# Kernel tuning notes

Hardware: AMD Instinct MI355X
Metric: run time of the kernel (lower is better)

## Reference

```python
import jax, jax.numpy as jnp
import numpy as np

# ---- architecture constants (from init_kwargs) ----
HID = 1024          # hidden_size
HK, HV = 4, 8       # linear_num_key_heads, linear_num_value_heads
DK, DV = 128, 128   # linear_key_head_dim, linear_value_head_dim
KEY_DIM = HK * DK   # 512
VAL_DIM = HV * DV   # 1024
CONV_DIM = 2 * KEY_DIM + VAL_DIM  # q,k,v concat -> 2048
KCONV = 4
NEXP, TOPK, INTER = 8, 2, 512
EPS = 1e-6


def setup_inputs() -> dict:
    key = jax.random.key(0)
    ks = jax.random.split(key, 12)
    def lin(k, shape, fan_in):
        return jax.random.normal(k, shape, jnp.float32) * (fan_in ** -0.5)
    return {
        "hidden_states": jax.random.normal(ks[0], (1, 2048, HID), jnp.float32),
        "w_ln1": jnp.zeros((HID,), jnp.float32),            # zero-centered RMSNorm weight
        "w_ln2": jnp.zeros((HID,), jnp.float32),
        "W_qkvz": lin(ks[1], (HID, 2 * KEY_DIM + 2 * VAL_DIM), HID),
        "W_ba": lin(ks[2], (HID, 2 * HV), HID),
        "conv_w": jax.random.normal(ks[3], (CONV_DIM, KCONV), jnp.float32) * (KCONV ** -0.5),
        "dt_bias": jax.random.normal(ks[4], (HV,), jnp.float32) * 0.1,
        "A_log": jnp.log(jax.random.uniform(ks[5], (HV,), jnp.float32, 1.0, 16.0)),
        "gate_norm_w": jnp.ones((DV,), jnp.float32),
        "W_out": lin(ks[6], (VAL_DIM, HID), VAL_DIM),
        "W_router": lin(ks[7], (HID, NEXP), HID),
        "W_gate_e": lin(ks[8], (NEXP, HID, INTER), HID),
        "W_up_e": lin(ks[9], (NEXP, HID, INTER), HID),
        "W_down_e": lin(ks[10], (NEXP, INTER, HID), INTER),
    }


def zrms(x, w):
    # zero-centered RMSNorm: effective weight is (1 + w)
    v = jnp.mean(x * x, axis=-1, keepdims=True)
    return x * jax.lax.rsqrt(v + EPS) * (1.0 + w)


def causal_dwconv(x, w):
    # x: [B,S,C], w: [C,K] depthwise causal conv
    xp = jnp.pad(x, ((0, 0), (KCONV - 1, 0), (0, 0)))
    kern = w.T[:, None, :]  # [K, 1, C] (HIO)
    return jax.lax.conv_general_dilated(
        xp, kern, (1,), 'VALID',
        dimension_numbers=('NHC', 'HIO', 'NHC'),
        feature_group_count=CONV_DIM)


def gated_delta_rule(q, k, v, g, beta):
    # q,k: [B,S,HV,DK] (l2-normed, q scaled); v: [B,S,HV,DV]; g,beta: [B,S,HV]
    B = q.shape[0]
    S0 = jnp.zeros((B, HV, DK, DV), q.dtype)
    def step(S, inp):
        qt, kt, vt, gt, bt = inp
        S = S * jnp.exp(gt)[..., None, None]
        kv = jnp.einsum('bhk,bhkv->bhv', kt, S)
        delta = (vt - kv) * bt[..., None]
        S = S + jnp.einsum('bhk,bhv->bhkv', kt, delta)
        o = jnp.einsum('bhk,bhkv->bhv', qt, S)
        return S, o
    xs = tuple(jnp.moveaxis(a, 1, 0) for a in (q, k, v, g, beta))
    _, o = jax.lax.scan(step, S0, xs)
    return jnp.moveaxis(o, 0, 1)  # [B,S,HV,DV]


def reference(hidden_states, w_ln1, w_ln2, W_qkvz, W_ba, conv_w, dt_bias, A_log,
              gate_norm_w, W_out, W_router, W_gate_e, W_up_e, W_down_e):
    B, S, _ = hidden_states.shape
    # ---- gated deltanet sub-block ----
    resid = hidden_states
    x = zrms(hidden_states, w_ln1)
    qkvz = x @ W_qkvz
    q, k, v, z = jnp.split(qkvz, [KEY_DIM, 2 * KEY_DIM, 2 * KEY_DIM + VAL_DIM], axis=-1)
    b, a = jnp.split(x @ W_ba, 2, axis=-1)            # each [B,S,HV]
    beta = jax.nn.sigmoid(b)
    g = -jnp.exp(A_log) * jax.nn.softplus(a + dt_bias)
    mixed = jnp.concatenate([q, k, v], axis=-1)
    mixed = jax.nn.silu(causal_dwconv(mixed, conv_w))
    q, k, v = jnp.split(mixed, [KEY_DIM, 2 * KEY_DIM], axis=-1)
    q = q.reshape(B, S, HK, DK)
    k = k.reshape(B, S, HK, DK)
    v = v.reshape(B, S, HV, DV)
    rep = HV // HK
    q = jnp.repeat(q, rep, axis=2)
    k = jnp.repeat(k, rep, axis=2)
    q = q * jax.lax.rsqrt(jnp.sum(q * q, -1, keepdims=True) + EPS)
    k = k * jax.lax.rsqrt(jnp.sum(k * k, -1, keepdims=True) + EPS)
    q = q * (DK ** -0.5)
    core = gated_delta_rule(q, k, v, g, beta)         # [B,S,HV,DV]
    # gated RMSNorm (per value head) with silu(z) gate
    core = core * jax.lax.rsqrt(jnp.mean(core * core, -1, keepdims=True) + EPS) * gate_norm_w
    core = core * jax.nn.silu(z.reshape(B, S, HV, DV))
    h = resid + core.reshape(B, S, VAL_DIM) @ W_out
    # ---- MoE sub-block ----
    resid = h
    x = zrms(h, w_ln2)
    probs = jax.nn.softmax(x @ W_router, axis=-1)     # [B,S,E]
    topv, topi = jax.lax.top_k(probs, TOPK)
    topv = topv / jnp.sum(topv, -1, keepdims=True)
    route = jnp.sum(jax.nn.one_hot(topi, NEXP, dtype=x.dtype) * topv[..., None], axis=-2)
    gate_h = jnp.einsum('bsh,ehi->bsei', x, W_gate_e)
    up_h = jnp.einsum('bsh,ehi->bsei', x, W_up_e)
    exp_out = jnp.einsum('bsei,eih->bseh', jax.nn.silu(gate_h) * up_h, W_down_e)
    moe_out = jnp.einsum('bseh,bse->bsh', exp_out, route)
    return (resid + moe_out, topi)
```

## Files before the change

### kernel.cpp

```cpp
#include <hip/hip_runtime.h>

#define S 2048
#define HID 1024
#define HK 4
#define HV 8
#define DK 128
#define DV 128
#define KEY_DIM 512
#define VAL_DIM 1024
#define CONV_DIM 2048
#define QKVZ_N 3072
#define NEXP 8
#define INTER 512
#define EPS 1e-6f
#define CK 64
#define NC 32

typedef unsigned short u16;
typedef unsigned int u32;
typedef __attribute__((ext_vector_type(8))) short bf16x8;
typedef __attribute__((ext_vector_type(4))) float f32x4;

__device__ __forceinline__ u16 f2b(float f) {
  u32 u = __builtin_bit_cast(u32, f);
  u += 0x7fff + ((u >> 16) & 1);
  return (u16)(u >> 16);
}

__device__ __forceinline__ void gload16(const u16* g, u16* l) {
  __builtin_amdgcn_global_load_lds(
      (const __attribute__((address_space(1))) void*)g,
      (__attribute__((address_space(3))) void*)l, 16, 0, 0);
}

__global__ __launch_bounds__(256) void k_rms(const float* __restrict__ x,
                                             const float* __restrict__ w,
                                             float* __restrict__ out,
                                             u16* __restrict__ outb) {
  const int row = blockIdx.x;
  const int tid = threadIdx.x;
  const float* xr = x + (size_t)row * HID;
  float4 v = ((const float4*)xr)[tid];
  float ss = v.x*v.x + v.y*v.y + v.z*v.z + v.w*v.w;
  for (int m = 1; m < 64; m <<= 1) ss += __shfl_xor(ss, m);
  __shared__ float sred[4];
  if ((tid & 63) == 0) sred[tid >> 6] = ss;
  __syncthreads();
  float tot = sred[0] + sred[1] + sred[2] + sred[3];
  float scale = 1.0f / sqrtf(tot * (1.0f / HID) + EPS);
  float4 wv = ((const float4*)w)[tid];
  float4 o;
  o.x = v.x * scale * (1.0f + wv.x);
  o.y = v.y * scale * (1.0f + wv.y);
  o.z = v.z * scale * (1.0f + wv.z);
  o.w = v.w * scale * (1.0f + wv.w);
  ((float4*)(out + (size_t)row * HID))[tid] = o;
  u32 p0 = (u32)f2b(o.x) | ((u32)f2b(o.y) << 16);
  u32 p1 = (u32)f2b(o.z) | ((u32)f2b(o.w) << 16);
  *(uint2*)&outb[(size_t)row * HID + tid * 4] = make_uint2(p0, p1);
}

__global__ __launch_bounds__(256) void k_transp(const float* __restrict__ src,
                                                u16* __restrict__ dst,
                                                int K, int N) {
  __shared__ float t[32][33];
  const size_t bo = (size_t)blockIdx.z * K * N;
  src += bo; dst += bo;
  int n0 = blockIdx.x * 32, k0 = blockIdx.y * 32;
  int tx = threadIdx.x & 31, ty = threadIdx.x >> 5;
#pragma unroll
  for (int i = 0; i < 32; i += 8)
    t[ty + i][tx] = src[(size_t)(k0 + ty + i) * N + n0 + tx];
  __syncthreads();
#pragma unroll
  for (int i = 0; i < 32; i += 8)
    dst[(size_t)(n0 + ty + i) * K + k0 + tx] = f2b(t[tx][ty + i]);
}

__global__ __launch_bounds__(256) void k_sgemm2(const float* __restrict__ A,
                                                const float* __restrict__ B,
                                                const float* __restrict__ Cadd,
                                                float* __restrict__ C,
                                                int M, int N, int K) {
  __shared__ float As[16][132];
  __shared__ float Bs[16][132];
  const int tid = threadIdx.x;
  const int ty = tid >> 4, tx = tid & 15;
  const int m0 = blockIdx.y * 128, n0 = blockIdx.x * 128;
  const int ar = tid >> 1, ak = (tid & 1) * 8;
  const int br = tid >> 4, bc = (tid & 15) * 8;
  float acc[8][8] = {};
  for (int k0 = 0; k0 < K; k0 += 16) {
    float4 a0 = *(const float4*)&A[(size_t)(m0 + ar) * K + k0 + ak];
    float4 a1 = *(const float4*)&A[(size_t)(m0 + ar) * K + k0 + ak + 4];
    As[ak + 0][ar] = a0.x; As[ak + 1][ar] = a0.y;
    As[ak + 2][ar] = a0.z; As[ak + 3][ar] = a0.w;
    As[ak + 4][ar] = a1.x; As[ak + 5][ar] = a1.y;
    As[ak + 6][ar] = a1.z; As[ak + 7][ar] = a1.w;
    *(float4*)&Bs[br][bc]     = *(const float4*)&B[(size_t)(k0 + br) * N + n0 + bc];
    *(float4*)&Bs[br][bc + 4] = *(const float4*)&B[(size_t)(k0 + br) * N + n0 + bc + 4];
    __syncthreads();
#pragma unroll
    for (int kk = 0; kk < 16; ++kk) {
      float4 aA = *(const float4*)&As[kk][ty * 8];
      float4 aB = *(const float4*)&As[kk][ty * 8 + 4];
      float4 bA = *(const float4*)&Bs[kk][tx * 8];
      float4 bB = *(const float4*)&Bs[kk][tx * 8 + 4];
      float a[8] = {aA.x, aA.y, aA.z, aA.w, aB.x, aB.y, aB.z, aB.w};
      float b[8] = {bA.x, bA.y, bA.z, bA.w, bB.x, bB.y, bB.z, bB.w};
#pragma unroll
      for (int i = 0; i < 8; ++i)
#pragma unroll
        for (int j = 0; j < 8; ++j) acc[i][j] += a[i] * b[j];
    }
    __syncthreads();
  }
#pragma unroll
  for (int i = 0; i < 8; ++i) {
    size_t off = (size_t)(m0 + ty * 8 + i) * N + n0 + tx * 8;
    float4 o0 = {acc[i][0], acc[i][1], acc[i][2], acc[i][3]};
    float4 o1 = {acc[i][4], acc[i][5], acc[i][6], acc[i][7]};
    if (Cadd) {
      float4 c0 = *(const float4*)&Cadd[off];
      float4 c1 = *(const float4*)&Cadd[off + 4];
      o0.x += c0.x; o0.y += c0.y; o0.z += c0.z; o0.w += c0.w;
      o1.x += c1.x; o1.y += c1.y; o1.z += c1.z; o1.w += c1.w;
    }
    *(float4*)&C[off] = o0;
    *(float4*)&C[off + 4] = o1;
  }
}

__global__ __launch_bounds__(256) void k_ba(const float* __restrict__ x1,
                                            const float* __restrict__ Wba,
                                            float* __restrict__ ba) {
  const int t = blockIdx.x, tid = threadIdx.x;
  const int n = tid >> 4, kl = tid & 15;
  const float* xr = x1 + (size_t)t * HID;
  float s = 0.f;
  for (int k = kl; k < HID; k += 16) s += xr[k] * Wba[k * 16 + n];
  for (int m = 1; m < 16; m <<= 1) s += __shfl_xor(s, m);
  if (kl == 0) ba[t * 16 + n] = s;
}

__global__ __launch_bounds__(256) void k_bg(const float* __restrict__ ba,
                                            const float* __restrict__ dt_bias,
                                            const float* __restrict__ A_log,
                                            float* __restrict__ gb,
                                            float* __restrict__ beta) {
  int i = blockIdx.x * 256 + threadIdx.x;
  if (i >= S * HV) return;
  int t = i >> 3, h = i & 7;
  float b = ba[t * 16 + h];
  float a = ba[t * 16 + 8 + h];
  beta[i] = 1.f / (1.f + expf(-b));
  float x = a + dt_bias[h];
  float sp = fmaxf(x, 0.f) + log1pf(expf(-fabsf(x)));
  gb[i] = -expf(A_log[h]) * sp;
}

__global__ __launch_bounds__(256) void k_conv(const float* __restrict__ qkvz,
                                              const float* __restrict__ cw,
                                              float* __restrict__ conv) {
  int idx = blockIdx.x * 256 + threadIdx.x;
  int t = idx >> 11, c = idx & 2047;
  float4 w = ((const float4*)cw)[c];
  float acc = 0.f;
  if (t >= 3) {
    acc = qkvz[(size_t)(t - 3) * QKVZ_N + c] * w.x
        + qkvz[(size_t)(t - 2) * QKVZ_N + c] * w.y
        + qkvz[(size_t)(t - 1) * QKVZ_N + c] * w.z
        + qkvz[(size_t)(t    ) * QKVZ_N + c] * w.w;
  } else {
    if (t - 3 >= 0) acc += qkvz[(size_t)(t - 3) * QKVZ_N + c] * w.x;
    if (t - 2 >= 0) acc += qkvz[(size_t)(t - 2) * QKVZ_N + c] * w.y;
    if (t - 1 >= 0) acc += qkvz[(size_t)(t - 1) * QKVZ_N + c] * w.z;
    acc += qkvz[(size_t)t * QKVZ_N + c] * w.w;
  }
  conv[idx] = acc / (1.f + expf(-acc));
}

__global__ __launch_bounds__(512) void k_prep(const float* __restrict__ conv,
                                              float* __restrict__ qn,
                                              float* __restrict__ kn) {
// ... 131 lines not shown
      *(float4*)&Upre[cb * 8192 + (size_t)(t0 + i) * 128 + c0 + 4] = o1;
    }
  }
  {
    const int r0 = (tid >> 3) * 4, t0 = (tid & 7) * 8;
    float acc[4][8] = {};
    for (int j = 0; j < 64; ++j) {
      float s = sW[j];
      float kk[4];
#pragma unroll
      for (int i = 0; i < 4; ++i) kk[i] = KT[r0 + i][j] * s;
      float m[8];
#pragma unroll
      for (int t = 0; t < 8; ++t) m[t] = Mm[t0 + t][j];
#pragma unroll
      for (int i = 0; i < 4; ++i)
#pragma unroll
        for (int t = 0; t < 8; ++t) acc[i][t] += kk[i] * m[t];
    }
#pragma unroll
    for (int i = 0; i < 4; ++i) {
      float4 o0 = {acc[i][0], acc[i][1], acc[i][2], acc[i][3]};
      float4 o1 = {acc[i][4], acc[i][5], acc[i][6], acc[i][7]};
      *(float4*)&WpT[cb * 8192 + (size_t)(r0 + i) * 64 + t0] = o0;
      *(float4*)&WpT[cb * 8192 + (size_t)(r0 + i) * 64 + t0 + 4] = o1;
    }
  }
  __syncthreads();

  float* QT = UB;
#pragma unroll
  for (int i = 0; i < 8; ++i) {
    int w = (i * 256 + tid) * 4;
    int tt = w >> 7, r = w & 127;
    float4 v = *(const float4*)&qn[(size_t)(t_base + tt) * 1024 + h * 128 + r];
    QT[(r + 0) * 68 + tt] = v.x; QT[(r + 1) * 68 + tt] = v.y;
    QT[(r + 2) * 68 + tt] = v.z; QT[(r + 3) * 68 + tt] = v.w;
  }
  __syncthreads();

  {
    const int t0 = (tid >> 4) * 4, j0 = (tid & 15) * 4;
    float acc[4][4] = {};
    for (int r = 0; r < 128; ++r) {
      float4 a = *(const float4*)&QT[r * 68 + t0];
      float4 b = *(const float4*)&KT[r][j0];
      float av[4] = {a.x, a.y, a.z, a.w};
      float bv[4] = {b.x, b.y, b.z, b.w};
#pragma unroll
      for (int i = 0; i < 4; ++i)
#pragma unroll
        for (int j = 0; j < 4; ++j) acc[i][j] += av[i] * bv[j];
    }
#pragma unroll
    for (int i = 0; i < 4; ++i)
#pragma unroll
      for (int j = 0; j < 4; ++j) {
        int t = t0 + i, jj = j0 + j;
        BqT[cb * 4096 + (size_t)jj * 64 + t] =
            (jj <= t) ? expf(c_l[t] - c_l[jj]) * acc[i][j] : 0.f;
      }
  }
#pragma unroll
  for (int i = 0; i < 8; ++i) {
    int w = (i * 256 + tid) * 4;
    int r = w >> 6, t = w & 63;
    float4 q = *(const float4*)&QT[r * 68 + t];
    float4 s = *(const float4*)&seQ[t];
    q.x *= s.x; q.y *= s.y; q.z *= s.z; q.w *= s.w;
    *(float4*)&Qdt[cb * 8192 + w] = q;
  }
#pragma unroll
  for (int i = 0; i < 8; ++i) {
    int w = (i * 256 + tid) * 4;
    int t = w >> 7, r = w & 127;
    float s = sKd[t];
    float4 o;
    o.x = KT[r + 0][t] * s; o.y = KT[r + 1][t] * s;
    o.z = KT[r + 2][t] * s; o.w = KT[r + 3][t] * s;
    *(float4*)&Kdm[cb * 8192 + w] = o;
  }
}

__global__ __launch_bounds__(256) void k_chunkB(
    const float* __restrict__ Upre, const float* __restrict__ WpT,
    const float* __restrict__ Qdt, const float* __restrict__ Kdm,
    const float* __restrict__ BqT, const float* __restrict__ dec,
    float* __restrict__ core) {
  const int h = blockIdx.x >> 3;
  const int cg = blockIdx.x & 7;
  const int cbase = cg * 16;
  const int tid = threadIdx.x;

  __shared__ float Sm[128][20];
  __shared__ float um[64][20];
  __shared__ float buf[128 * 68];
  __shared__ float Bs[64][68];

  for (int i = tid; i < 128 * 20; i += 256) (&Sm[0][0])[i] = 0.f;

  const int t0 = (tid >> 3) * 2;
  const int cc = (tid & 7) * 2;
  const int r0 = (tid >> 3) * 4;
  __syncthreads();

  for (int ch = 0; ch < NC; ++ch) {
    const size_t cb = (size_t)h * NC + ch;
    const float* Wp = WpT + cb * 8192;
    const float* Qp = Qdt + cb * 8192;
    const float* Kp = Kdm + cb * 8192;
    const float* Up = Upre + cb * 8192;
    const float* Bp = BqT + cb * 4096;
    const float dC = dec[cb];

#pragma unroll
    for (int i = 0; i < 8; ++i) {
      int w = (i * 256 + tid) * 4;
      *(float4*)&buf[(w >> 6) * 68 + (w & 63)] = *(const float4*)&Wp[w];
    }
#pragma unroll
    for (int i = 0; i < 4; ++i) {
      int w = (i * 256 + tid) * 4;
      *(float4*)&Bs[w >> 6][w & 63] = *(const float4*)&Bp[w];
    }
    __syncthreads();

    {
      float a00 = 0, a01 = 0, a10 = 0, a11 = 0;
#pragma unroll 4
      for (int r = 0; r < 128; ++r) {
        float2 wv = *(const float2*)&buf[r * 68 + t0];
        float2 sv = *(const float2*)&Sm[r][cc];
        a00 += wv.x * sv.x; a01 += wv.x * sv.y;
        a10 += wv.y * sv.x; a11 += wv.y * sv.y;
      }
      float2 u0 = *(const float2*)&Up[(size_t)t0 * 128 + cbase + cc];
      float2 u1 = *(const float2*)&Up[(size_t)(t0 + 1) * 128 + cbase + cc];
      u0.x -= a00; u0.y -= a01;
      u1.x -= a10; u1.y -= a11;
      *(float2*)&um[t0][cc] = u0;
      *(float2*)&um[t0 + 1][cc] = u1;
    }
    __syncthreads();

#pragma unroll
    for (int i = 0; i < 8; ++i) {
      int w = (i * 256 + tid) * 4;
      *(float4*)&buf[(w >> 6) * 68 + (w & 63)] = *(const float4*)&Qp[w];
    }
    __syncthreads();

    {
      float a00 = 0, a01 = 0, a10 = 0, a11 = 0;
#pragma unroll 4
      for (int r = 0; r < 128; ++r) {
        float2 qv = *(const float2*)&buf[r * 68 + t0];
        float2 sv = *(const float2*)&Sm[r][cc];
        a00 += qv.x * sv.x; a01 += qv.x * sv.y;
        a10 += qv.y * sv.x; a11 += qv.y * sv.y;
      }
#pragma unroll 4
      for (int j = 0; j < 64; ++j) {
        float2 bv = *(const float2*)&Bs[j][t0];
        float2 uv = *(const float2*)&um[j][cc];
        a00 += bv.x * uv.x; a01 += bv.x * uv.y;
        a10 += bv.y * uv.x; a11 += bv.y * uv.y;
      }
      float2 o0 = {a00, a01}, o1 = {a10, a11};
      *(float2*)&core[(size_t)(ch * 64 + t0) * 1024 + h * 128 + cbase + cc] = o0;
      *(float2*)&core[(size_t)(ch * 64 + t0 + 1) * 1024 + h * 128 + cbase + cc] = o1;
    }
    __syncthreads();

#pragma unroll
    for (int i = 0; i < 8; ++i) {
      int w = (i * 256 + tid) * 4;
      *(float4*)&buf[(w >> 7) * 132 + (w & 127)] = *(const float4*)&Kp[w];
    }
    __syncthreads();

    {
      float acc[4][2] = {};
#pragma unroll 2
      for (int t = 0; t < 64; ++t) {
        float4 kv = *(const float4*)&buf[t * 132 + r0];
        float2 uv = *(const float2*)&um[t][cc];
        acc[0][0] += kv.x * uv.x; acc[0][1] += kv.x * uv.y;
        acc[1][0] += kv.y * uv.x; acc[1][1] += kv.y * uv.y;
        acc[2][0] += kv.z * uv.x; acc[2][1] += kv.z * uv.y;
        acc[3][0] += kv.w * uv.x; acc[3][1] += kv.w * uv.y;
      }
#pragma unroll
      for (int i = 0; i < 4; ++i) {
        float2 s = *(const float2*)&Sm[r0 + i][cc];
        s.x = dC * s.x + acc[i][0];
        s.y = dC * s.y + acc[i][1];
        *(float2*)&Sm[r0 + i][cc] = s;
      }
    }
    __syncthreads();
  }
}

__global__ __launch_bounds__(256) void k_gatenorm(const float* __restrict__ core,
                                                  const float* __restrict__ qkvz,
                                                  const float* __restrict__ gnw,
                                                  float* __restrict__ y) {
  const int t = blockIdx.x, tid = threadIdx.x;
  const int wave = tid >> 6, lane = tid & 63;
  const int h = blockIdx.y * 4 + wave;
  const float* cbp = core + (size_t)t * 1024 + h * DV;
  float c0 = cbp[lane], c1 = cbp[lane + 64];
  float ss = c0 * c0 + c1 * c1;
  for (int m = 1; m < 64; m <<= 1) ss += __shfl_xor(ss, m);
  float scale = 1.f / sqrtf(ss * (1.0f / DV) + EPS);
  const float* zb = qkvz + (size_t)t * QKVZ_N + 2 * KEY_DIM + VAL_DIM + h * DV;
  float z0 = zb[lane], z1 = zb[lane + 64];
  float g0 = gnw[lane], g1 = gnw[lane + 64];
  float o0 = c0 * scale * g0 * (z0 / (1.f + expf(-z0)));
  float o1 = c1 * scale * g1 * (z1 / (1.f + expf(-z1)));
  float* yb = y + (size_t)t * 1024 + h * DV;
  yb[lane] = o0; yb[lane + 64] = o1;
}

__global__ __launch_bounds__(256) void k_router(const float* __restrict__ x2,
                                                const float* __restrict__ Wr,
                                                float* __restrict__ rinfo,
                                                int* __restrict__ cnt,
                                                float* __restrict__ outTopi) {
  const int t = blockIdx.x, tid = threadIdx.x;
  const int n = tid >> 5, kl = tid & 31;
  const float* xr = x2 + (size_t)t * HID;
  float s = 0.f;
  for (int k = kl; k < HID; k += 32) s += xr[k] * Wr[k * 8 + n];
  for (int m = 1; m < 32; m <<= 1) s += __shfl_xor(s, m);
  __shared__ float lg[8];
  if (kl == 0) lg[n] = s;
  __syncthreads();
  if (tid == 0) {
    int i0 = 0; float m0 = lg[0];
    for (int e = 1; e < 8; ++e) if (lg[e] > m0) { m0 = lg[e]; i0 = e; }
    int i1 = -1; float m1 = -1e30f;
    for (int e = 0; e < 8; ++e) if (e != i0 && lg[e] > m1) { m1 = lg[e]; i1 = e; }
    float e1 = expf(m1 - m0);
    float w0 = 1.f / (1.f + e1);
    float w1 = e1 / (1.f + e1);
    rinfo[t * 4 + 0] = (float)i0; rinfo[t * 4 + 1] = (float)i1;
    rinfo[t * 4 + 2] = w0;        rinfo[t * 4 + 3] = w1;
    atomicAdd(&cnt[i0], 1);
    atomicAdd(&cnt[i1], 1);
    outTopi[t * 2 + 0] = (float)i0;
    outTopi[t * 2 + 1] = (float)i1;
  }
}

__global__ void k_offsets(const int* __restrict__ cnt, int* __restrict__ offs,
                          int* __restrict__ cnt2) {
  if (threadIdx.x == 0) {
    int a = 0;
    for (int e = 0; e < 8; ++e) { offs[e] = a; a += cnt[e]; cnt2[e] = 0; }
  }
}

__global__ __launch_bounds__(256) void k_scatter(const float* __restrict__ rinfo,
                                                 const int* __restrict__ offs,
                                                 int* __restrict__ cnt2,
                                                 int* __restrict__ pairTok,
                                                 int* __restrict__ tokPos) {
  int t = blockIdx.x * 256 + threadIdx.x;
  if (t >= S) return;
  int i0 = (int)rinfo[t * 4 + 0], i1 = (int)rinfo[t * 4 + 1];
  int p0 = offs[i0] + atomicAdd(&cnt2[i0], 1);
  pairTok[p0] = t;
  int p1 = offs[i1] + atomicAdd(&cnt2[i1], 1);
  pairTok[p1] = t;
  tokPos[t * 2 + 0] = p0;
  tokPos[t * 2 + 1] = p1;
}

__global__ __launch_bounds__(256) void k_moe1m(const u16* __restrict__ x2b,
                                               const u16* __restrict__ WgT,
                                               const u16* __restrict__ WuT,
                                               const int* __restrict__ offs,
// ... 94 lines not shown
  for (int k0 = 0; k0 < 512; k0 += 32) {
    gload16(Ag0 + k0, Abuf + wb0);
    gload16(Ag1 + k0, Abuf + wb1);
    gload16(Bg0 + k0, Bbuf + wb0);
    gload16(Bg1 + k0, Bbuf + wb1);
    __syncthreads();
    bf16x8 af[4], bfr[4];
#pragma unroll
    for (int i = 0; i < 4; ++i) {
      af[i]  = *(const bf16x8*)&Abuf[(wm * 64 + i * 16 + fr) * 32 + kg * 8];
      bfr[i] = *(const bf16x8*)&Bbuf[(wn * 64 + i * 16 + fr) * 32 + kg * 8];
    }
#pragma unroll
    for (int i = 0; i < 4; ++i)
#pragma unroll
      for (int j = 0; j < 4; ++j)
        acc[i][j] = __builtin_amdgcn_mfma_f32_16x16x32_bf16(af[i], bfr[j], acc[i][j], 0, 0, 0);
    __syncthreads();
  }
#pragma unroll
  for (int i = 0; i < 4; ++i) {
#pragma unroll
    for (int j = 0; j < 4; ++j) {
      int rowt = wm * 64 + i * 16 + kg * 4;
      int col = n0 + wn * 64 + j * 16 + fr;
#pragma unroll
      for (int r = 0; r < 4; ++r) {
        if (m0 + rowt + r < count)
          eo[(size_t)(base + m0 + rowt + r) * 1024 + col] = acc[i][j][r];
      }
    }
  }
}

__global__ __launch_bounds__(256) void k_finish(const float* __restrict__ eo,
                                                const int* __restrict__ tokPos,
                                                const float* __restrict__ rinfo,
                                                float* __restrict__ out) {
  const int t = blockIdx.x;
  const int c = threadIdx.x * 4;
  float w0 = rinfo[t * 4 + 2], w1 = rinfo[t * 4 + 3];
  int p0 = tokPos[t * 2 + 0], p1 = tokPos[t * 2 + 1];
  float4 a = *(const float4*)&eo[(size_t)p0 * 1024 + c];
  float4 b = *(const float4*)&eo[(size_t)p1 * 1024 + c];
  float4 o = *(const float4*)&out[(size_t)t * 1024 + c];
  o.x += w0 * a.x + w1 * b.x;
  o.y += w0 * a.y + w1 * b.y;
  o.z += w0 * a.z + w1 * b.z;
  o.w += w0 * a.w + w1 * b.w;
  *(float4*)&out[(size_t)t * 1024 + c] = o;
}

extern "C" void kernel_launch(void* const* d_in, const int* in_sizes, int n_in,
                              void* d_out, int out_size, void* d_ws, size_t ws_size,
                              hipStream_t stream) {
  const float* hid      = (const float*)d_in[0];
  const float* w_ln1    = (const float*)d_in[1];
  const float* w_ln2    = (const float*)d_in[2];
  const float* W_qkvz   = (const float*)d_in[3];
  const float* W_ba     = (const float*)d_in[4];
  const float* conv_w   = (const float*)d_in[5];
  const float* dt_bias  = (const float*)d_in[6];
  const float* A_log    = (const float*)d_in[7];
  const float* gnw      = (const float*)d_in[8];
  const float* W_out    = (const float*)d_in[9];
  const float* W_router = (const float*)d_in[10];
  const float* W_gate   = (const float*)d_in[11];
  const float* W_up     = (const float*)d_in[12];
  const float* W_down   = (const float*)d_in[13];

  float* ws = (float*)d_ws;
  const size_t M1 = (size_t)1024 * 1024;
  float* x1    = ws;
  float* qkvz  = x1 + 2 * M1;
  float* conv  = qkvz + 6 * M1;
  float* qn    = conv + 4 * M1;
  float* kn    = qn + 2 * M1;
  float* core  = kn + 2 * M1;
  float* Upre  = core + 2 * M1;
  float* WpT   = Upre + 2 * M1;
  float* Qdt   = WpT + 2 * M1;
  float* Kdm   = Qdt + 2 * M1;
  float* BqT   = Kdm + 2 * M1;
  float* dec   = BqT + M1;
  float* ba    = dec + 256;
  float* gb    = ba + 32768;
  float* betab = gb + 16384;
  float* rinfo = betab + 16384;
  int*   ints  = (int*)(rinfo + 8192);
  int* cnt     = ints;
  int* cnt2    = ints + 8;
  int* offs    = ints + 16;
  int* pairTok = ints + 32;
  int* tokPos  = ints + 4128;
  u16* x1b     = (u16*)(ints + 8224);

  u16* WgT = (u16*)conv;
  u16* WuT = (u16*)(conv + 2 * M1);
  u16* WdT = (u16*)kn;
  u16* act = (u16*)Kdm;
  float* eo = Upre;

  float* outF = (float*)d_out;
  const size_t N1 = (size_t)S * HID;

  hipMemsetAsync(cnt, 0, 16 * sizeof(int), stream);

  k_rms<<<S, 256, 0, stream>>>(hid, w_ln1, x1, x1b);
  k_sgemm2<<<dim3(24, 16), 256, 0, stream>>>(x1, W_qkvz, nullptr, qkvz, S, QKVZ_N, HID);
  k_ba<<<S, 256, 0, stream>>>(x1, W_ba, ba);
  k_bg<<<(S * HV + 255) / 256, 256, 0, stream>>>(ba, dt_bias, A_log, gb, betab);
  k_conv<<<(S * CONV_DIM) / 256, 256, 0, stream>>>(qkvz, conv_w, conv);
  k_prep<<<S, 512, 0, stream>>>(conv, qn, kn);
  k_chunkA<<<HV * NC, 256, 0, stream>>>(qn, kn, conv, gb, betab,
                                        Upre, WpT, Qdt, Kdm, BqT, dec);
  k_transp<<<dim3(16, 32, 8), 256, 0, stream>>>(W_gate, WgT, 1024, 512);
  k_transp<<<dim3(16, 32, 8), 256, 0, stream>>>(W_up, WuT, 1024, 512);
  k_transp<<<dim3(32, 16, 8), 256, 0, stream>>>(W_down, WdT, 512, 1024);
  k_chunkB<<<64, 256, 0, stream>>>(Upre, WpT, Qdt, Kdm, BqT, dec, core);
  k_gatenorm<<<dim3(S, 2), 256, 0, stream>>>(core, qkvz, gnw, core);
  k_sgemm2<<<dim3(8, 16), 256, 0, stream>>>(core, W_out, hid, outF, S, HID, VAL_DIM);
  k_rms<<<S, 256, 0, stream>>>(outF, w_ln2, x1, x1b);
  k_router<<<S, 256, 0, stream>>>(x1, W_router, rinfo, cnt, outF + N1);
  k_offsets<<<1, 64, 0, stream>>>(cnt, offs, cnt2);
  k_scatter<<<(S + 255) / 256, 256, 0, stream>>>(rinfo, offs, cnt2, pairTok, tokPos);
  k_moe1m<<<dim3(4, 32, 8), 256, 0, stream>>>(x1b, WgT, WuT, offs, cnt, pairTok, act);
  k_moe2m<<<dim3(8, 32, 8), 256, 0, stream>>>(act, WdT, offs, cnt, eo);
  k_finish<<<S, 256, 0, stream>>>(eo, tokPos, rinfo, outF);
}
```

Baseline: 1.133 ms.

## Split chunked delta-rule into serial state pass and parallel output kernel

The sequential chunk kernel is split in two. The first (64 blocks) only carries the recurrent state across chunks, saving the per-chunk state snapshot to scratch buffers and prefetching the next chunk's W and K tiles into registers. The second runs the output computation for all 8x32x8 chunk tiles in parallel from those snapshots. The SGEMM also gains register double-buffering of its global loads. In exchange, the U-correction matmul is now computed twice and extra scratch traffic is added, and the snapshots reuse the x1/qn buffers as storage.

```diff
diff --git a/kernel.cpp b/kernel.cpp
--- a/kernel.cpp
+++ b/kernel.cpp
@@ -90,16 +90,25 @@
   const int ar = tid >> 1, ak = (tid & 1) * 8;
   const int br = tid >> 4, bc = (tid & 15) * 8;
   float acc[8][8] = {};
+  float4 ra0, ra1, rb0, rb1;
+  ra0 = *(const float4*)&A[(size_t)(m0 + ar) * K + ak];
+  ra1 = *(const float4*)&A[(size_t)(m0 + ar) * K + ak + 4];
+  rb0 = *(const float4*)&B[(size_t)br * N + n0 + bc];
+  rb1 = *(const float4*)&B[(size_t)br * N + n0 + bc + 4];
   for (int k0 = 0; k0 < K; k0 += 16) {
-    float4 a0 = *(const float4*)&A[(size_t)(m0 + ar) * K + k0 + ak];
-    float4 a1 = *(const float4*)&A[(size_t)(m0 + ar) * K + k0 + ak + 4];
-    As[ak + 0][ar] = a0.x; As[ak + 1][ar] = a0.y;
-    As[ak + 2][ar] = a0.z; As[ak + 3][ar] = a0.w;
-    As[ak + 4][ar] = a1.x; As[ak + 5][ar] = a1.y;
-    As[ak + 6][ar] = a1.z; As[ak + 7][ar] = a1.w;
-    *(float4*)&Bs[br][bc]     = *(const float4*)&B[(size_t)(k0 + br) * N + n0 + bc];
-    *(float4*)&Bs[br][bc + 4] = *(const float4*)&B[(size_t)(k0 + br) * N + n0 + bc + 4];
+    As[ak + 0][ar] = ra0.x; As[ak + 1][ar] = ra0.y;
+    As[ak + 2][ar] = ra0.z; As[ak + 3][ar] = ra0.w;
+    As[ak + 4][ar] = ra1.x; As[ak + 5][ar] = ra1.y;
+    As[ak + 6][ar] = ra1.z; As[ak + 7][ar] = ra1.w;
+    *(float4*)&Bs[br][bc]     = rb0;
+    *(float4*)&Bs[br][bc + 4] = rb1;
     __syncthreads();
+    if (k0 + 16 < K) {
+      ra0 = *(const float4*)&A[(size_t)(m0 + ar) * K + k0 + 16 + ak];
+      ra1 = *(const float4*)&A[(size_t)(m0 + ar) * K + k0 + 16 + ak + 4];
+      rb0 = *(const float4*)&B[(size_t)(k0 + 16 + br) * N + n0 + bc];
+      rb1 = *(const float4*)&B[(size_t)(k0 + 16 + br) * N + n0 + bc + 4];
+    }
 #pragma unroll
     for (int kk = 0; kk < 16; ++kk) {
       float4 aA = *(const float4*)&As[kk][ty * 8];
@@ -397,11 +406,10 @@
   }
 }
 
-__global__ __launch_bounds__(256) void k_chunkB(
+__global__ __launch_bounds__(256) void k_chunkS(
     const float* __restrict__ Upre, const float* __restrict__ WpT,
-    const float* __restrict__ Qdt, const float* __restrict__ Kdm,
-    const float* __restrict__ BqT, const float* __restrict__ dec,
-    float* __restrict__ core) {
+    const float* __restrict__ Kdm, const float* __restrict__ dec,
+    float* __restrict__ Schk0, float* __restrict__ Schk1) {
   const int h = blockIdx.x >> 3;
   const int cg = blockIdx.x & 7;
   const int cbase = cg * 16;
@@ -409,42 +417,69 @@
 
   __shared__ float Sm[128][20];
   __shared__ float um[64][20];
-  __shared__ float buf[128 * 68];
-  __shared__ float Bs[64][68];
+  __shared__ float bufW[128 * 68];
+  __shared__ float bufK[64 * 132];
 
   for (int i = tid; i < 128 * 20; i += 256) (&Sm[0][0])[i] = 0.f;
+
+  float* Sc_base = (h < 4) ? (Schk0 + (size_t)(h * 8 + cg) * NC * 2048)
+                           : (Schk1 + (size_t)((h - 4) * 8 + cg) * NC * 2048);
 
   const int t0 = (tid >> 3) * 2;
   const int cc = (tid & 7) * 2;
   const int r0 = (tid >> 3) * 4;
+  const int sr = tid >> 1, sc = (tid & 1) * 8;
+
+  float4 pw[8], pk[8];
+  {
+    const float* Wp = WpT + (size_t)h * NC * 8192;
+    const float* Kp = Kdm + (size_t)h * NC * 8192;
+#pragma unroll
+    for (int i = 0; i < 8; ++i) {
+      int w = (i * 256 + tid) * 4;
+      pw[i] = *(const float4*)&Wp[w];
+      pk[i] = *(const float4*)&Kp[w];
+    }
+  }
   __syncthreads();
 
   for (int ch = 0; ch < NC; ++ch) {
     const size_t cb = (size_t)h * NC + ch;
-    const float* Wp = WpT + cb * 8192;
-    const float* Qp = Qdt + cb * 8192;
-    const float* Kp = Kdm + cb * 8192;
     const float* Up = Upre + cb * 8192;
-    const float* Bp = BqT + cb * 4096;
     const float dC = dec[cb];
 
 #pragma unroll
     for (int i = 0; i < 8; ++i) {
       int w = (i * 256 + tid) * 4;
-      *(float4*)&buf[(w >> 6) * 68 + (w & 63)] = *(const float4*)&Wp[w];
-    }
-#pragma unroll
-    for (int i = 0; i < 4; ++i) {
-      int w = (i * 256 + tid) * 4;
-      *(float4*)&Bs[w >> 6][w & 63] = *(const float4*)&Bp[w];
+      *(float4*)&bufW[(w >> 6) * 68 + (w & 63)] = pw[i];
+      *(float4*)&bufK[(w >> 7) * 132 + (w & 127)] = pk[i];
     }
     __syncthreads();
+
+    if (ch + 1 < NC) {
+      const float* Wp = WpT + (cb + 1) * 8192;
+      const float* Kp = Kdm + (cb + 1) * 8192;
+#pragma unroll
+      for (int i = 0; i < 8; ++i) {
+        int w = (i * 256 + tid) * 4;
+        pw[i] = *(const float4*)&Wp[w];
+        pk[i] = *(const float4*)&Kp[w];
+      }
+    }
+
+    {
+      float* Sc = Sc_base + (size_t)ch * 2048;
+      float4 s0 = *(const float4*)&Sm[sr][sc];
+      float4 s1 = *(const float4*)&Sm[sr][sc + 4];
+      *(float4*)&Sc[tid * 8] = s0;
+      *(float4*)&Sc[tid * 8 + 4] = s1;
+    }
 
     {
       float a00 = 0, a01 = 0, a10 = 0, a11 = 0;
 #pragma unroll 4
       for (int r = 0; r < 128; ++r) {
-        float2 wv = *(const float2*)&buf[r * 68 + t0];
+        float2 wv = *(const float2*)&bufW[r * 68 + t0];
         float2 sv = *(const float2*)&Sm[r][cc];
         a00 += wv.x * sv.x; a01 += wv.x * sv.y;
         a10 += wv.y * sv.x; a11 += wv.y * sv.y;
@@ -458,47 +493,11 @@
     }
     __syncthreads();
 
-#pragma unroll
-    for (int i = 0; i < 8; ++i) {
-      int w = (i * 256 + tid) * 4;
-      *(float4*)&buf[(w >> 6) * 68 + (w & 63)] = *(const float4*)&Qp[w];
-    }
-    __syncthreads();
-
-    {
-      float a00 = 0, a01 = 0, a10 = 0, a11 = 0;
-#pragma unroll 4
-      for (int r = 0; r < 128; ++r) {
-        float2 qv = *(const float2*)&buf[r * 68 + t0];
-        float2 sv = *(const float2*)&Sm[r][cc];
-        a00 += qv.x * sv.x; a01 += qv.x * sv.y;
-        a10 += qv.y * sv.x; a11 += qv.y * sv.y;
-      }
-#pragma unroll 4
-      for (int j = 0; j < 64; ++j) {
-        float2 bv = *(const float2*)&Bs[j][t0];
-        float2 uv = *(const float2*)&um[j][cc];
-        a00 += bv.x * uv.x; a01 += bv.x * uv.y;
-        a10 += bv.y * uv.x; a11 += bv.y * uv.y;
-      }
-      float2 o0 = {a00, a01}, o1 = {a10, a11};
-      *(float2*)&core[(size_t)(ch * 64 + t0) * 1024 + h * 128 + cbase + cc] = o0;
-      *(float2*)&core[(size_t)(ch * 64 + t0 + 1) * 1024 + h * 128 + cbase + cc] = o1;
-    }
-    __syncthreads();
-
-#pragma unroll
-    for (int i = 0; i < 8; ++i) {
-      int w = (i * 256 + tid) * 4;
-      *(float4*)&buf[(w >> 7) * 132 + (w & 127)] = *(const float4*)&Kp[w];
-    }
-    __syncthreads();
-
     {
       float acc[4][2] = {};
 #pragma unroll 2
       for (int t = 0; t < 64; ++t) {
-        float4 kv = *(const float4*)&buf[t * 132 + r0];
+        float4 kv = *(const float4*)&bufK[t * 132 + r0];
         float2 uv = *(const float2*)&um[t][cc];
         acc[0][0] += kv.x * uv.x; acc[0][1] += kv.x * uv.y;
         acc[1][0] += kv.y * uv.x; acc[1][1] += kv.y * uv.y;
@@ -514,6 +513,104 @@
       }
     }
     __syncthreads();
+  }
+}
+
+__global__ __launch_bounds__(256) void k_chunkO(
+    const float* __restrict__ Upre, const float* __restrict__ WpT,
+    const float* __restrict__ Qdt, const float* __restrict__ BqT,
+    const float* __restrict__ Schk0, const float* __restrict__ Schk1,
+    float* __restrict__ core) {
+  const int cg = blockIdx.x;
+  const int ch = blockIdx.y;
+  const int h = blockIdx.z;
+  const int cbase = cg * 16;
+  const int tid = threadIdx.x;
+
+  __shared__ float Sm[128][20];
+  __shared__ float um[64][20];
+  __shared__ float buf[128 * 68];
+  __shared__ float Bs[64][68];
+
+  const size_t cb = (size_t)h * NC + ch;
+  const float* Up = Upre + cb * 8192;
+  const float* Sc = ((h < 4) ? (Schk0 + (size_t)(h * 8 + cg) * NC * 2048)
+                             : (Schk1 + (size_t)((h - 4) * 8 + cg) * NC * 2048))
+                    + (size_t)ch * 2048;
+
+  {
+    const int sr = tid >> 1, sc2 = (tid & 1) * 8;
+    float4 s0 = *(const float4*)&Sc[tid * 8];
+    float4 s1 = *(const float4*)&Sc[tid * 8 + 4];
+    *(float4*)&Sm[sr][sc2] = s0;
+    *(float4*)&Sm[sr][sc2 + 4] = s1;
+  }
+  {
+    const float* Wp = WpT + cb * 8192;
+    const float* Bp = BqT + cb * 4096;
+#pragma unroll
+    for (int i = 0; i < 8; ++i) {
+      int w = (i * 256 + tid) * 4;
+      *(float4*)&buf[(w >> 6) * 68 + (w & 63)] = *(const float4*)&Wp[w];
+    }
+#pragma unroll
+    for (int i = 0; i < 4; ++i) {
+      int w = (i * 256 + tid) * 4;
+      *(float4*)&Bs[w >> 6][w & 63] = *(const float4*)&Bp[w];
+    }
+  }
+  __syncthreads();
+
+  const int t0 = (tid >> 3) * 2;
+  const int cc = (tid & 7) * 2;
+
+  {
+    float a00 = 0, a01 = 0, a10 = 0, a11 = 0;
+#pragma unroll 4
+    for (int r = 0; r < 128; ++r) {
+      float2 wv = *(const float2*)&buf[r * 68 + t0];
+      float2 sv = *(const float2*)&Sm[r][cc];
+      a00 += wv.x * sv.x; a01 += wv.x * sv.y;
+      a10 += wv.y * sv.x; a11 += wv.y * sv.y;
+    }
+    float2 u0 = *(const float2*)&Up[(size_t)t0 * 128 + cbase + cc];
+    float2 u1 = *(const float2*)&Up[(size_t)(t0 + 1) * 128 + cbase + cc];
+    u0.x -= a00; u0.y -= a01;
+    u1.x -= a10; u1.y -= a11;
+    *(float2*)&um[t0][cc] = u0;
+    *(float2*)&um[t0 + 1][cc] = u1;
+  }
+  __syncthreads();
+
+  {
+    const float* Qp = Qdt + cb * 8192;
+#pragma unroll
+    for (int i = 0; i < 8; ++i) {
+      int w = (i * 256 + tid) * 4;
+      *(float4*)&buf[(w >> 6) * 68 + (w & 63)] = *(const float4*)&Qp[w];
+    }
+  }
+  __syncthreads();
+
+  {
+    float a00 = 0, a01 = 0, a10 = 0, a11 = 0;
+#pragma unroll 4
+    for (int r = 0; r < 128; ++r) {
+      float2 qv = *(const float2*)&buf[r * 68 + t0];
+      float2 sv = *(const float2*)&Sm[r][cc];
+      a00 += qv.x * sv.x; a01 += qv.x * sv.y;
+      a10 += qv.y * sv.x; a11 += qv.y * sv.y;
+    }
+#pragma unroll 4
+    for (int j = 0; j < 64; ++j) {
+      float2 bv = *(const float2*)&Bs[j][t0];
+      float2 uv = *(const float2*)&um[j][cc];
+      a00 += bv.x * uv.x; a01 += bv.x * uv.y;
+      a10 += bv.y * uv.x; a11 += bv.y * uv.y;
+    }
+    float2 o0 = {a00, a01}, o1 = {a10, a11};
+    *(float2*)&core[(size_t)(ch * 64 + t0) * 1024 + h * 128 + cbase + cc] = o0;
+    *(float2*)&core[(size_t)(ch * 64 + t0 + 1) * 1024 + h * 128 + cbase + cc] = o1;
   }
 }
 
@@ -792,6 +889,8 @@
   u16* WdT = (u16*)kn;
   u16* act = (u16*)Kdm;
   float* eo = Upre;
+  float* Schk0 = x1;
+  float* Schk1 = qn;
 
   float* outF = (float*)d_out;
   const size_t N1 = (size_t)S * HID;
@@ -809,7 +908,8 @@
   k_transp<<<dim3(16, 32, 8), 256, 0, stream>>>(W_gate, WgT, 1024, 512);
   k_transp<<<dim3(16, 32, 8), 256, 0, stream>>>(W_up, WuT, 1024, 512);
   k_transp<<<dim3(32, 16, 8), 256, 0, stream>>>(W_down, WdT, 512, 1024);
-  k_chunkB<<<64, 256, 0, stream>>>(Upre, WpT, Qdt, Kdm, BqT, dec, core);
+  k_chunkS<<<64, 256, 0, stream>>>(Upre, WpT, Kdm, dec, Schk0, Schk1);
+  k_chunkO<<<dim3(8, 32, 8), 256, 0, stream>>>(Upre, WpT, Qdt, BqT, Schk0, Schk1, core);
   k_gatenorm<<<dim3(S, 2), 256, 0, stream>>>(core, qkvz, gnw, core);
   k_sgemm2<<<dim3(8, 16), 256, 0, stream>>>(core, W_out, hid, outF, S, HID, VAL_DIM);
   k_rms<<<S, 256, 0, stream>>>(outF, w_ln2, x1, x1b);
```

Measured after the change: 1.086 ms. 1.04x faster.

## Split chunked delta-rule into transition build, serial state scan, and parallel output

Applied to the files above, without the earlier changes.

The serial per-chunk loop (which recomputed the state update and the output inside one 64-block kernel) is split into three kernels. The first builds a per-chunk transition matrix T = dI - K·W and an additive term from U. The second runs a lightweight serial scan S ← T·S + b that stores every chunk's starting state. The third computes outputs for all chunks in parallel across a much larger grid. The fp32 GEMM also gains register prefetch of the next K tile. This exposes more parallelism than the latency-bound serial kernel, at the cost of extra workspace traffic (16K floats per chunk for T, b and the states) and reusing workspace buffers, which carries aliasing risk.

```diff
diff --git a/kernel.cpp b/kernel.cpp
--- a/kernel.cpp
+++ b/kernel.cpp
@@ -90,16 +90,25 @@
   const int ar = tid >> 1, ak = (tid & 1) * 8;
   const int br = tid >> 4, bc = (tid & 15) * 8;
   float acc[8][8] = {};
+  float4 ra0, ra1, rb0, rb1;
+  ra0 = *(const float4*)&A[(size_t)(m0 + ar) * K + ak];
+  ra1 = *(const float4*)&A[(size_t)(m0 + ar) * K + ak + 4];
+  rb0 = *(const float4*)&B[(size_t)br * N + n0 + bc];
+  rb1 = *(const float4*)&B[(size_t)br * N + n0 + bc + 4];
   for (int k0 = 0; k0 < K; k0 += 16) {
-    float4 a0 = *(const float4*)&A[(size_t)(m0 + ar) * K + k0 + ak];
-    float4 a1 = *(const float4*)&A[(size_t)(m0 + ar) * K + k0 + ak + 4];
-    As[ak + 0][ar] = a0.x; As[ak + 1][ar] = a0.y;
-    As[ak + 2][ar] = a0.z; As[ak + 3][ar] = a0.w;
-    As[ak + 4][ar] = a1.x; As[ak + 5][ar] = a1.y;
-    As[ak + 6][ar] = a1.z; As[ak + 7][ar] = a1.w;
-    *(float4*)&Bs[br][bc]     = *(const float4*)&B[(size_t)(k0 + br) * N + n0 + bc];
-    *(float4*)&Bs[br][bc + 4] = *(const float4*)&B[(size_t)(k0 + br) * N + n0 + bc + 4];
+    As[ak + 0][ar] = ra0.x; As[ak + 1][ar] = ra0.y;
+    As[ak + 2][ar] = ra0.z; As[ak + 3][ar] = ra0.w;
+    As[ak + 4][ar] = ra1.x; As[ak + 5][ar] = ra1.y;
+    As[ak + 6][ar] = ra1.z; As[ak + 7][ar] = ra1.w;
+    *(float4*)&Bs[br][bc]     = rb0;
+    *(float4*)&Bs[br][bc + 4] = rb1;
     __syncthreads();
+    if (k0 + 16 < K) {
+      ra0 = *(const float4*)&A[(size_t)(m0 + ar) * K + k0 + 16 + ak];
+      ra1 = *(const float4*)&A[(size_t)(m0 + ar) * K + k0 + 16 + ak + 4];
+      rb0 = *(const float4*)&B[(size_t)(k0 + 16 + br) * N + n0 + bc];
+      rb1 = *(const float4*)&B[(size_t)(k0 + 16 + br) * N + n0 + bc + 4];
+    }
 #pragma unroll
     for (int kk = 0; kk < 16; ++kk) {
       float4 aA = *(const float4*)&As[kk][ty * 8];
@@ -397,13 +406,122 @@
   }
 }
 
-__global__ __launch_bounds__(256) void k_chunkB(
+__global__ __launch_bounds__(256) void k_chunkT(
+    const float* __restrict__ WpT, const float* __restrict__ Kdm,
+    const float* __restrict__ Upre, const float* __restrict__ dec,
+    float* __restrict__ Tc, float* __restrict__ bcb) {
+  const int mode = blockIdx.x;
+  const int ch = blockIdx.y;
+  const int h = blockIdx.z;
+  const int tid = threadIdx.x;
+  const size_t cb = (size_t)h * NC + ch;
+  const int rbase = (mode & 1) * 64;
+  const bool isT = mode < 2;
+  __shared__ float Ms[64 * 132];
+  if (isT) {
+#pragma unroll
+    for (int i = 0; i < 8; ++i) {
+      int idx = i * 256 + tid;
+      int k = idx >> 4;
+      int t0 = (idx & 15) * 4;
+      float4 v = *(const float4*)&WpT[cb * 8192 + (size_t)k * 64 + t0];
+      Ms[(t0 + 0) * 132 + k] = v.x;
+      Ms[(t0 + 1) * 132 + k] = v.y;
+      Ms[(t0 + 2) * 132 + k] = v.z;
+      Ms[(t0 + 3) * 132 + k] = v.w;
+    }
+  } else {
+#pragma unroll
+    for (int i = 0; i < 8; ++i) {
+      int idx = i * 256 + tid;
+      int t = idx >> 5;
+      int c0 = (idx & 31) * 4;
+      *(float4*)&Ms[t * 132 + c0] =
+          *(const float4*)&Upre[cb * 8192 + (size_t)t * 128 + c0];
+    }
+  }
+  __syncthreads();
+  const int rr = rbase + (tid >> 4) * 4;
+  const int m0 = (tid & 15) * 8;
+  float acc[4][8] = {};
+#pragma unroll 2
+  for (int t = 0; t < 64; ++t) {
+    float4 kd = *(const float4*)&Kdm[cb * 8192 + (size_t)t * 128 + rr];
+    float kv[4] = {kd.x, kd.y, kd.z, kd.w};
+    float4 ma = *(const float4*)&Ms[t * 132 + m0];
+    float4 mb = *(const float4*)&Ms[t * 132 + m0 + 4];
+    float mv[8] = {ma.x, ma.y, ma.z, ma.w, mb.x, mb.y, mb.z, mb.w};
+#pragma unroll
+    for (int i = 0; i < 4; ++i)
+#pragma unroll
+      for (int j = 0; j < 8; ++j) acc[i][j] += kv[i] * mv[j];
+  }
+  if (isT) {
+    const float dC = dec[cb];
+#pragma unroll
+    for (int j = 0; j < 8; ++j) {
+      int k = m0 + j;
+      float4 v;
+      v.x = ((rr + 0) == k ? dC : 0.f) - acc[0][j];
+      v.y = ((rr + 1) == k ? dC : 0.f) - acc[1][j];
+      v.z = ((rr + 2) == k ? dC : 0.f) - acc[2][j];
+      v.w = ((rr + 3) == k ? dC : 0.f) - acc[3][j];
+      *(float4*)&Tc[cb * 16384 + (size_t)k * 128 + rr] = v;
+    }
+  } else {
+#pragma unroll
+    for (int j = 0; j < 8; ++j) {
+      float4 v = {acc[0][j], acc[1][j], acc[2][j], acc[3][j]};
+      *(float4*)&bcb[cb * 16384 + (size_t)(m0 + j) * 128 + rr] = v;
+    }
+  }
+}
+
+__global__ __launch_bounds__(256) void k_chunkS2(
+    const float* __restrict__ Tc, const float* __restrict__ bcb,
+    float* __restrict__ Sg0, float* __restrict__ Sg1) {
+  const int h = blockIdx.x >> 4;
+  const int cg = blockIdx.x & 15;
+  const int tid = threadIdx.x;
+  const int cl = tid & 7;
+  const int cglob = cg * 8 + cl;
+  const int r0 = (tid >> 3) * 4;
+  __shared__ float Sm[128 * 9];
+  float s0 = 0.f, s1 = 0.f, s2 = 0.f, s3 = 0.f;
+  Sm[(r0 + 0) * 9 + cl] = 0.f; Sm[(r0 + 1) * 9 + cl] = 0.f;
+  Sm[(r0 + 2) * 9 + cl] = 0.f; Sm[(r0 + 3) * 9 + cl] = 0.f;
+  __syncthreads();
+  float* Sgb = (h < 4) ? (Sg0 + (size_t)h * NC * 16384)
+                       : (Sg1 + (size_t)(h - 4) * NC * 16384);
+  for (int ch = 0; ch < NC; ++ch) {
+    const size_t cb = (size_t)h * NC + ch;
+    float4 sv = {s0, s1, s2, s3};
+    *(float4*)&Sgb[(size_t)ch * 16384 + (size_t)cglob * 128 + r0] = sv;
+    float4 a = *(const float4*)&bcb[cb * 16384 + (size_t)cglob * 128 + r0];
+    float a0 = a.x, a1 = a.y, a2 = a.z, a3 = a.w;
+    const float* Tp = Tc + cb * 16384;
+#pragma unroll 4
+    for (int k = 0; k < 128; ++k) {
+      float4 tv = *(const float4*)&Tp[(size_t)k * 128 + r0];
+      float skc = Sm[k * 9 + cl];
+      a0 += tv.x * skc; a1 += tv.y * skc; a2 += tv.z * skc; a3 += tv.w * skc;
+    }
+    __syncthreads();
+    Sm[(r0 + 0) * 9 + cl] = a0; Sm[(r0 + 1) * 9 + cl] = a1;
+    Sm[(r0 + 2) * 9 + cl] = a2; Sm[(r0 + 3) * 9 + cl] = a3;
+    s0 = a0; s1 = a1; s2 = a2; s3 = a3;
+    __syncthreads();
+  }
+}
+
+__global__ __launch_bounds__(256) void k_chunkO(
     const float* __restrict__ Upre, const float* __restrict__ WpT,
-    const float* __restrict__ Qdt, const float* __restrict__ Kdm,
-    const float* __restrict__ BqT, const float* __restrict__ dec,
+    const float* __restrict__ Qdt, const float* __restrict__ BqT,
+    const float* __restrict__ Sg0, const float* __restrict__ Sg1,
     float* __restrict__ core) {
-  const int h = blockIdx.x >> 3;
-  const int cg = blockIdx.x & 7;
+  const int cg = blockIdx.x;
+  const int ch = blockIdx.y;
+  const int h = blockIdx.z;
   const int cbase = cg * 16;
   const int tid = threadIdx.x;
 
@@ -412,22 +530,25 @@
   __shared__ float buf[128 * 68];
   __shared__ float Bs[64][68];
 
-  for (int i = tid; i < 128 * 20; i += 256) (&Sm[0][0])[i] = 0.f;
-
-  const int t0 = (tid >> 3) * 2;
-  const int cc = (tid & 7) * 2;
-  const int r0 = (tid >> 3) * 4;
-  __syncthreads();
-
-  for (int ch = 0; ch < NC; ++ch) {
-    const size_t cb = (size_t)h * NC + ch;
+  const size_t cb = (size_t)h * NC + ch;
+  const float* Up = Upre + cb * 8192;
+  const float* Sc = ((h < 4) ? (Sg0 + (size_t)h * NC * 16384)
+                             : (Sg1 + (size_t)(h - 4) * NC * 16384))
+                    + (size_t)ch * 16384;
+
+  {
+    int c = tid & 15;
+    int rr = (tid >> 4) * 8;
+    float4 v0 = *(const float4*)&Sc[(size_t)(cbase + c) * 128 + rr];
+    float4 v1 = *(const float4*)&Sc[(size_t)(cbase + c) * 128 + rr + 4];
+    Sm[rr + 0][c] = v0.x; Sm[rr + 1][c] = v0.y;
+    Sm[rr + 2][c] = v0.z; Sm[rr + 3][c] = v0.w;
+    Sm[rr + 4][c] = v1.x; Sm[rr + 5][c] = v1.y;
+    Sm[rr + 6][c] = v1.z; Sm[rr + 7][c] = v1.w;
+  }
+  {
     const float* Wp = WpT + cb * 8192;
-    const float* Qp = Qdt + cb * 8192;
-    const float* Kp = Kdm + cb * 8192;
-    const float* Up = Upre + cb * 8192;
     const float* Bp = BqT + cb * 4096;
-    const float dC = dec[cb];
-
 #pragma unroll
     for (int i = 0; i < 8; ++i) {
       int w = (i * 256 + tid) * 4;
@@ -438,82 +559,59 @@
       int w = (i * 256 + tid) * 4;
       *(float4*)&Bs[w >> 6][w & 63] = *(const float4*)&Bp[w];
     }
-    __syncthreads();
-
-    {
-      float a00 = 0, a01 = 0, a10 = 0, a11 = 0;
+  }
+  __syncthreads();
+
+  const int t0 = (tid >> 3) * 2;
+  const int cc = (tid & 7) * 2;
+
+  {
+    float a00 = 0, a01 = 0, a10 = 0, a11 = 0;
 #pragma unroll 4
-      for (int r = 0; r < 128; ++r) {
-        float2 wv = *(const float2*)&buf[r * 68 + t0];
-        float2 sv = *(const float2*)&Sm[r][cc];
-        a00 += wv.x * sv.x; a01 += wv.x * sv.y;
-        a10 += wv.y * sv.x; a11 += wv.y * sv.y;
-      }
-      float2 u0 = *(const float2*)&Up[(size_t)t0 * 128 + cbase + cc];
-      float2 u1 = *(const float2*)&Up[(size_t)(t0 + 1) * 128 + cbase + cc];
-      u0.x -= a00; u0.y -= a01;
-      u1.x -= a10; u1.y -= a11;
-      *(float2*)&um[t0][cc] = u0;
-      *(float2*)&um[t0 + 1][cc] = u1;
-    }
-    __syncthreads();
-
+    for (int r = 0; r < 128; ++r) {
+      float2 wv = *(const float2*)&buf[r * 68 + t0];
+      float2 sv = *(const float2*)&Sm[r][cc];
+      a00 += wv.x * sv.x; a01 += wv.x * sv.y;
+      a10 += wv.y * sv.x; a11 += wv.y * sv.y;
+    }
+    float2 u0 = *(const float2*)&Up[(size_t)t0 * 128 + cbase + cc];
+    float2 u1 = *(const float2*)&Up[(size_t)(t0 + 1) * 128 + cbase + cc];
+    u0.x -= a00; u0.y -= a01;
+    u1.x -= a10; u1.y -= a11;
+    *(float2*)&um[t0][cc] = u0;
+    *(float2*)&um[t0 + 1][cc] = u1;
+  }
+  __syncthreads();
+
+  {
+    const float* Qp = Qdt + cb * 8192;
 #pragma unroll
     for (int i = 0; i < 8; ++i) {
       int w = (i * 256 + tid) * 4;
       *(float4*)&buf[(w >> 6) * 68 + (w & 63)] = *(const float4*)&Qp[w];
     }
-    __syncthreads();
-
-    {
-      float a00 = 0, a01 = 0, a10 = 0, a11 = 0;
+  }
+  __syncthreads();
+
+  {
+    float a00 = 0, a01 = 0, a10 = 0, a11 = 0;
 #pragma unroll 4
-      for (int r = 0; r < 128; ++r) {
-        float2 qv = *(const float2*)&buf[r * 68 + t0];
-        float2 sv = *(const float2*)&Sm[r][cc];
-        a00 += qv.x * sv.x; a01 += qv.x * sv.y;
-        a10 += qv.y * sv.x; a11 += qv.y * sv.y;
-      }
+    for (int r = 0; r < 128; ++r) {
+      float2 qv = *(const float2*)&buf[r * 68 + t0];
+      float2 sv = *(const float2*)&Sm[r][cc];
+      a00 += qv.x * sv.x; a01 += qv.x * sv.y;
+      a10 += qv.y * sv.x; a11 += qv.y * sv.y;
+    }
 #pragma unroll 4
-      for (int j = 0; j < 64; ++j) {
-        float2 bv = *(const float2*)&Bs[j][t0];
-        float2 uv = *(const float2*)&um[j][cc];
-        a00 += bv.x * uv.x; a01 += bv.x * uv.y;
-        a10 += bv.y * uv.x; a11 += bv.y * uv.y;
-      }
-      float2 o0 = {a00, a01}, o1 = {a10, a11};
-      *(float2*)&core[(size_t)(ch * 64 + t0) * 1024 + h * 128 + cbase + cc] = o0;
-      *(float2*)&core[(size_t)(ch * 64 + t0 + 1) * 1024 + h * 128 + cbase + cc] = o1;
-    }
-    __syncthreads();
-
-#pragma unroll
-    for (int i = 0; i < 8; ++i) {
-      int w = (i * 256 + tid) * 4;
-      *(float4*)&buf[(w >> 7) * 132 + (w & 127)] = *(const float4*)&Kp[w];
-    }
-    __syncthreads();
-
-    {
-      float acc[4][2] = {};
-#pragma unroll 2
-      for (int t = 0; t < 64; ++t) {
-        float4 kv = *(const float4*)&buf[t * 132 + r0];
-        float2 uv = *(const float2*)&um[t][cc];
-        acc[0][0] += kv.x * uv.x; acc[0][1] += kv.x * uv.y;
-        acc[1][0] += kv.y * uv.x; acc[1][1] += kv.y * uv.y;
-        acc[2][0] += kv.z * uv.x; acc[2][1] += kv.z * uv.y;
-        acc[3][0] += kv.w * uv.x; acc[3][1] += kv.w * uv.y;
-      }
-#pragma unroll
-      for (int i = 0; i < 4; ++i) {
-        float2 s = *(const float2*)&Sm[r0 + i][cc];
-        s.x = dC * s.x + acc[i][0];
-        s.y = dC * s.y + acc[i][1];
-        *(float2*)&Sm[r0 + i][cc] = s;
-      }
-    }
-    __syncthreads();
+    for (int j = 0; j < 64; ++j) {
+      float2 bv = *(const float2*)&Bs[j][t0];
+      float2 uv = *(const float2*)&um[j][cc];
+      a00 += bv.x * uv.x; a01 += bv.x * uv.y;
+      a10 += bv.y * uv.x; a11 += bv.y * uv.y;
+    }
+    float2 o0 = {a00, a01}, o1 = {a10, a11};
+    *(float2*)&core[(size_t)(ch * 64 + t0) * 1024 + h * 128 + cbase + cc] = o0;
+    *(float2*)&core[(size_t)(ch * 64 + t0 + 1) * 1024 + h * 128 + cbase + cc] = o1;
   }
 }
 
@@ -774,7 +872,8 @@
   float* Qdt   = WpT + 2 * M1;
   float* Kdm   = Qdt + 2 * M1;
   float* BqT   = Kdm + 2 * M1;
-  float* dec   = BqT + M1;
+  float* Sg1   = BqT + M1;
+  float* dec   = Sg1 + 2 * M1;
   float* ba    = dec + 256;
   float* gb    = ba + 32768;
   float* betab = gb + 16384;
@@ -787,6 +886,9 @@
   int* tokPos  = ints + 4128;
   u16* x1b     = (u16*)(ints + 8224);
 
+  float* Tc  = conv;
+  float* bcb = qn;
+  float* Sg0 = x1;
   u16* WgT = (u16*)conv;
   u16* WuT = (u16*)(conv + 2 * M1);
   u16* WdT = (u16*)kn;
@@ -806,10 +908,12 @@
   k_prep<<<S, 512, 0, stream>>>(conv, qn, kn);
   k_chunkA<<<HV * NC, 256, 0, stream>>>(qn, kn, conv, gb, betab,
                                         Upre, WpT, Qdt, Kdm, BqT, dec);
+  k_chunkT<<<dim3(4, 32, 8), 256, 0, stream>>>(WpT, Kdm, Upre, dec, Tc, bcb);
+  k_chunkS2<<<128, 256, 0, stream>>>(Tc, bcb, Sg0, Sg1);
   k_transp<<<dim3(16, 32, 8), 256, 0, stream>>>(W_gate, WgT, 1024, 512);
   k_transp<<<dim3(16, 32, 8), 256, 0, stream>>>(W_up, WuT, 1024, 512);
   k_transp<<<dim3(32, 16, 8), 256, 0, stream>>>(W_down, WdT, 512, 1024);
-  k_chunkB<<<64, 256, 0, stream>>>(Upre, WpT, Qdt, Kdm, BqT, dec, core);
+  k_chunkO<<<dim3(8, 32, 8), 256, 0, stream>>>(Upre, WpT, Qdt, BqT, Sg0, Sg1, core);
   k_gatenorm<<<dim3(S, 2), 256, 0, stream>>>(core, qkvz, gnw, core);
   k_sgemm2<<<dim3(8, 16), 256, 0, stream>>>(core, W_out, hid, outF, S, HID, VAL_DIM);
   k_rms<<<S, 256, 0, stream>>>(outF, w_ln2, x1, x1b);
```

Measured after the change: 1.129 ms. Within noise of the previous version (-0.4%).
